# Performance work log

Measured on AMD Instinct MI355X. Metric: run time of the kernel, lower is better.

## Reference

```python
import jax, jax.numpy as jnp
import numpy as np

B, T, E = 4, 2048, 2048
NH, NKV, HD = 16, 4, 128
THETA = 10000.0


def _rope(x, pos_ids, theta):
    # x: [b, h, t, hd]; pos_ids: [b, t]; theta: [hd/2]
    ang = pos_ids[:, None, :, None].astype(jnp.float32) * theta  # [b,1,t,hd/2]
    cos, sin = jnp.cos(ang), jnp.sin(ang)
    x1, x2 = x[..., ::2], x[..., 1::2]
    # interleave rotated pairs back to [..., hd]
    rot = jnp.stack([x1 * cos - x2 * sin, x1 * sin + x2 * cos], axis=-1)
    return rot.reshape(x.shape)


def setup_inputs() -> dict:
    key = jax.random.key(0)
    ks = jax.random.split(key, 10)
    s = 0.02
    x = jax.random.normal(ks[0], (B, T, E), dtype=jnp.float32)
    attention_mask = jax.random.randint(ks[1], (B, T, T), 0, 2, dtype=jnp.int32)
    # torch nn.Linear weights stored here as [in, out] (y = x @ W + b)
    Wq = jax.random.normal(ks[2], (E, E), dtype=jnp.float32) * s
    bq = jnp.zeros((E,), dtype=jnp.float32)
    Wk = jax.random.normal(ks[3], (E, NKV * HD), dtype=jnp.float32) * s
    bk = jnp.zeros((NKV * HD,), dtype=jnp.float32)
    Wv = jax.random.normal(ks[4], (E, NKV * HD), dtype=jnp.float32) * s
    bv = jnp.zeros((NKV * HD,), dtype=jnp.float32)
    Wo = jax.random.normal(ks[5], (E, E), dtype=jnp.float32) * s
    bo = jnp.zeros((E,), dtype=jnp.float32)
    return {"x": x, "attention_mask": attention_mask, "Wq": Wq, "bq": bq,
            "Wk": Wk, "bk": bk, "Wv": Wv, "bv": bv, "Wo": Wo, "bo": bo}


def reference(x, attention_mask, Wq, bq, Wk, bk, Wv, bv, Wo, bo):
    b, t = x.shape[0], x.shape[1]
    # faithful to original: plain reshape (view), NOT transpose-based head split
    q = (x @ Wq + bq).reshape(b, NH, t, HD)
    k = (x @ Wk + bk).reshape(b, NKV, t, HD)
    v = (x @ Wv + bv).reshape(b, NKV, t, HD)
    theta = THETA ** (-jnp.arange(0, HD, 2, dtype=jnp.float32) / HD)
    pos = jnp.broadcast_to(jnp.arange(t), (b, t))
    # original RoPE.forward is wrapped in @torch.no_grad() -> stop_gradient
    k = jax.lax.stop_gradient(_rope(k, pos, theta))
    v = jax.lax.stop_gradient(_rope(v, pos, theta))  # note: RoPE applied to V too
    g = NH // NKV
    k = jnp.tile(k, (1, g, 1, 1))  # torch .repeat tiles kv heads
    v = jnp.tile(v, (1, g, 1, 1))
    # original divides by head_dim ** (-0.5) == multiply by sqrt(head_dim)
    scores = jnp.einsum('bhqd,bhkd->bhqk', q, k) * (HD ** 0.5)
    scores = jnp.where(attention_mask[:, None, :, :] == 0, jnp.float32(1e-9), scores)
    attn = jax.nn.softmax(scores, axis=-1)  # dropout inactive (eval mode)
    out = jnp.einsum('bhqk,bhkd->bhqd', attn, v)
    out = out.transpose(0, 2, 1, 3).reshape(b, t, NH * HD)
    return out @ Wo + bo
```

## Files before the change

kernel.cpp:

```cpp
#include <hip/hip_runtime.h>
#include <math.h>

constexpr int Bc   = 4;
constexpr int Tc   = 2048;
constexpr int Ec   = 2048;
constexpr int NHc  = 16;
constexpr int NKVc = 4;
constexpr int HDc  = 128;
constexpr int KVEc = NKVc * HDc;

typedef __attribute__((ext_vector_type(8))) short bf16x8;
typedef __attribute__((ext_vector_type(4))) short short4v;
typedef __attribute__((ext_vector_type(4))) float f32x4;

__device__ __forceinline__ short f2bf(float f) {
    union { float f; unsigned u; } v; v.f = f;
    unsigned r = v.u + 0x7FFF + ((v.u >> 16) & 1);
    return (short)(r >> 16);
}
__device__ __forceinline__ float bf2f(short s) {
    union { unsigned u; float f; } v; v.u = ((unsigned)(unsigned short)s) << 16;
    return v.f;
}
__device__ __forceinline__ void gload16(const void* g, void* l) {
    __builtin_amdgcn_global_load_lds(
        (const __attribute__((address_space(1))) unsigned*)g,
        (__attribute__((address_space(3))) unsigned*)l, 16, 0, 0);
}

__global__ __launch_bounds__(256)
void convert_split(const float* __restrict__ X, short* __restrict__ Xhi,
                   short* __restrict__ Xlo)
{
    int i = blockIdx.x * 256 + threadIdx.x;
    float4 v = ((const float4*)X)[i];
    float fv[4] = {v.x, v.y, v.z, v.w};
    short4v hi, lo;
    #pragma unroll
    for (int j = 0; j < 4; ++j) {
        hi[j] = f2bf(fv[j]);
        lo[j] = f2bf(fv[j] - bf2f(hi[j]));
    }
    ((short4v*)Xhi)[i] = hi;
    ((short4v*)Xlo)[i] = lo;
}

__global__ __launch_bounds__(256)
void transpose_split(const float* __restrict__ W, short* __restrict__ WThi,
                     short* __restrict__ WTlo, int K, int N)
{
    __shared__ float Ls[32][33];
    const int k0 = blockIdx.x * 32, n0 = blockIdx.y * 32;
    const int t = threadIdx.x;
    const int r = t >> 3, c4 = (t & 7) << 2;
    float4 v = *(const float4*)(W + (size_t)(k0 + r) * N + n0 + c4);
    Ls[r][c4 + 0] = v.x; Ls[r][c4 + 1] = v.y;
    Ls[r][c4 + 2] = v.z; Ls[r][c4 + 3] = v.w;
    __syncthreads();
    short4v hi, lo;
    #pragma unroll
    for (int i = 0; i < 4; ++i) {
        float f = Ls[c4 + i][r];
        hi[i] = f2bf(f);
        lo[i] = f2bf(f - bf2f(hi[i]));
    }
    *(short4v*)(WThi + (size_t)(n0 + r) * K + k0 + c4) = hi;
    if (WTlo) *(short4v*)(WTlo + (size_t)(n0 + r) * K + k0 + c4) = lo;
}

__global__ __launch_bounds__(256)
void mask_bits(const int* __restrict__ mask, unsigned long long* __restrict__ Mb)
{
    const int widx = blockIdx.x * 4 + (threadIdx.x >> 6);
    const int L = threadIdx.x & 63;
    const int m = mask[(size_t)widx * 64 + L];
    unsigned long long bits = __ballot(m != 0);
    if (L == 0) Mb[widx] = bits;
}

template <bool SPLIT>
__global__ __launch_bounds__(256, 2)
void gemm_mfma(const short* __restrict__ Ahi, const short* __restrict__ Alo,
               const short* __restrict__ Bhi, const short* __restrict__ Blo,
               const float* __restrict__ bias, float* __restrict__ C,
               int M, int N, int K)
{
    __shared__ short AsH[128 * 32];
    __shared__ short BsH[128 * 32];
    __shared__ short AsL[SPLIT ? 128 * 32 : 8];
    __shared__ short BsL[SPLIT ? 128 * 32 : 8];

    const int t = threadIdx.x;
    const int w = t >> 6, L = t & 63;
    const int l16 = L & 15, quad = L >> 4;
    const int wr = w >> 1, wc = w & 1;
    const int bm = blockIdx.x * 128, bn = blockIdx.y * 128;

    const int sm = L >> 2;
    const int sq = ((L & 3) - (sm >> 2)) & 3;
    const int scol = sq * 8;

    f32x4 acc[4][4];
    #pragma unroll
    for (int mi = 0; mi < 4; ++mi)
        #pragma unroll
        for (int ni = 0; ni < 4; ++ni) acc[mi][ni] = (f32x4){0, 0, 0, 0};

    const int fxor = (quad + (l16 >> 2)) & 3;

    for (int k0 = 0; k0 < K; k0 += 32) {
        __syncthreads();
        #pragma unroll
        for (int i = 0; i < 2; ++i) {
            const int wl = w * 2 + i;
            const size_t ra = (size_t)(bm + wl * 16 + sm) * K + k0 + scol;
            const size_t rb = (size_t)(bn + wl * 16 + sm) * K + k0 + scol;
            gload16(Ahi + ra, &AsH[wl * 512]);
            gload16(Bhi + rb, &BsH[wl * 512]);
            if (SPLIT) {
                gload16(Alo + ra, &AsL[wl * 512]);
                gload16(Blo + rb, &BsL[wl * 512]);
            }
        }
        __syncthreads();

        bf16x8 ah[4], bh[4], al[4], bl[4];
        #pragma unroll
        for (int mi = 0; mi < 4; ++mi) {
            const int ch = ((wr * 4 + mi) * 64 + l16 * 4 + fxor) * 8;
            ah[mi] = *(const bf16x8*)&AsH[ch];
            if (SPLIT) al[mi] = *(const bf16x8*)&AsL[ch];
        }
        #pragma unroll
        for (int ni = 0; ni < 4; ++ni) {
            const int ch = ((wc * 4 + ni) * 64 + l16 * 4 + fxor) * 8;
            bh[ni] = *(const bf16x8*)&BsH[ch];
            if (SPLIT) bl[ni] = *(const bf16x8*)&BsL[ch];
        }
        #pragma unroll
        for (int mi = 0; mi < 4; ++mi)
            #pragma unroll
            for (int ni = 0; ni < 4; ++ni) {
                acc[mi][ni] = __builtin_amdgcn_mfma_f32_16x16x32_bf16(
                    ah[mi], bh[ni], acc[mi][ni], 0, 0, 0);
                if (SPLIT) {
                    acc[mi][ni] = __builtin_amdgcn_mfma_f32_16x16x32_bf16(
                        al[mi], bh[ni], acc[mi][ni], 0, 0, 0);
                    acc[mi][ni] = __builtin_amdgcn_mfma_f32_16x16x32_bf16(
                        ah[mi], bl[ni], acc[mi][ni], 0, 0, 0);
                }
            }
    }

    #pragma unroll
    for (int ni = 0; ni < 4; ++ni) {
        const int col = bn + wc * 64 + ni * 16 + l16;
        const float bv = bias[col];
        #pragma unroll
        for (int mi = 0; mi < 4; ++mi) {
            #pragma unroll
            for (int r = 0; r < 4; ++r) {
                const int row = bm + wr * 64 + mi * 16 + quad * 4 + r;
                C[(size_t)row * N + col] = acc[mi][ni][r] + bv;
            }
        }
    }
}

__global__ __launch_bounds__(256)
void rope_k(const float* __restrict__ X2d, short* __restrict__ Khi,
            short* __restrict__ Klo)
{
    const int idx = blockIdx.x * 256 + threadIdx.x;
    const int j  = idx & 63;
    const int tk = (idx >> 6) & (Tc - 1);
    const int kh = (idx >> 17) & (NKVc - 1);
    const int bb = idx >> 19;
    const int row = (kh << 9) + (tk >> 2);
    const int col = ((tk & 3) << 7) + (j << 1);
    const float* src = X2d + ((size_t)bb * Tc + row) * KVEc + col;
    const float a = src[0];
    const float b = src[1];
    const float theta = powf(10000.0f, -(float)j * (1.0f / 64.0f));
    const float ang = (float)tk * theta;
    float s, c;
    sincosf(ang, &s, &c);
    const float r0 = a * c - b * s;
    const float r1 = a * s + b * c;
    const size_t off = (((size_t)bb * NKVc + kh) * Tc + tk) * HDc + (j << 1);
    short h0 = f2bf(r0), h1 = f2bf(r1);
    Khi[off]     = h0;  Klo[off]     = f2bf(r0 - bf2f(h0));
    Khi[off + 1] = h1;  Klo[off + 1] = f2bf(r1 - bf2f(h1));
}

__global__ __launch_bounds__(256)
void rope_v_t(const float* __restrict__ V2d, short* __restrict__ Vt)
{
    __shared__ short Ls[128][40];
    const int g  = blockIdx.x;
    const int kh = blockIdx.y;
    const int bb = blockIdx.z;
    const int t  = threadIdx.x;

    const float* src = V2d + ((size_t)bb * Tc + (kh << 9) + (g << 3)) * KVEc;
    #pragma unroll
    for (int i = 0; i < 4; ++i) {
        int e = i * 256 + t;
        float4 v = ((const float4*)src)[e];
        int row = e >> 7;
        int col = (e & 127) << 2;
        int tkl = (row << 2) + (col >> 7);
        int d0  = col & 127;
        int tk  = (g << 5) + tkl;
        float fv[4] = {v.x, v.y, v.z, v.w};
        #pragma unroll
        for (int p = 0; p < 2; ++p) {
            int j = (d0 >> 1) + p;
            float theta = powf(10000.0f, -(float)j * (1.0f / 64.0f));
            float ang = (float)tk * theta;
            float s, c;
            sincosf(ang, &s, &c);
            float a = fv[2 * p], b = fv[2 * p + 1];
            Ls[d0 + 2 * p    ][tkl] = f2bf(a * c - b * s);
            Ls[d0 + 2 * p + 1][tkl] = f2bf(a * s + b * c);
        }
    }
    __syncthreads();
    const int d = t >> 1;
    const int h16 = (t & 1) << 4;
    short* dst = Vt + (((size_t)bb * NKVc + kh) * HDc + d) * Tc + (g << 5) + h16;
    bf16x8 o0 = *(const bf16x8*)&Ls[d][h16];
    bf16x8 o1 = *(const bf16x8*)&Ls[d][h16 + 8];
    *(bf16x8*)dst = o0;
    *(bf16x8*)(dst + 8) = o1;
}

__global__ __launch_bounds__(256, 2)
void attn_mfma(const float* __restrict__ Q2d, const short* __restrict__ Khi_g,
               const short* __restrict__ Klo_g, const short* __restrict__ Vt_g,
               const unsigned long long* __restrict__ Mb, short* __restrict__ AObf)
{
    constexpr int SP = 72;
    __shared__ short KhiS[64 * 128];
    __shared__ short KloS[64 * 128];
    __shared__ short VtS [128 * 64];
    __shared__ short Ps  [64 * SP];

    const int qb = blockIdx.x;
    const int h  = blockIdx.y;
    const int bb = blockIdx.z;
    const int t  = threadIdx.x;
    const int w    = t >> 6;
    const int L    = t & 63;
    const int l16  = L & 15;
    const int quad = L >> 4;
    const int kh   = h & (NKVc - 1);
    const int tq0  = qb * 64 + w * 16;

    bf16x8 qhi[4], qlo[4];
    {
        const float* qrow = Q2d +
            ((size_t)(bb * Tc + h * HDc + qb * 4 + w)) * Ec + 128 * l16;
        #pragma unroll
        for (int kc = 0; kc < 4; ++kc) {
            const float* p = qrow + kc * 32 + quad * 8;
            #pragma unroll
            for (int j = 0; j < 8; ++j) {
                float f = p[j];
                short hi = f2bf(f);
                qhi[kc][j] = hi;
                qlo[kc][j] = f2bf(f - bf2f(hi));
            }
        }
    }

    float m_r[4], lp[4];
    #pragma unroll
    for (int r = 0; r < 4; ++r) { m_r[r] = -INFINITY; lp[r] = 0.0f; }
    f32x4 o[8];
    #pragma unroll
    for (int nc = 0; nc < 8; ++nc) o[nc] = (f32x4){0, 0, 0, 0};

    const short* kbh = Khi_g + ((size_t)(bb * NKVc + kh)) * Tc * HDc;
    const short* kbl = Klo_g + ((size_t)(bb * NKVc + kh)) * Tc * HDc;
    const short* vb  = Vt_g  + ((size_t)(bb * NKVc + kh)) * HDc * Tc;
    const unsigned long long* mrow0 =
        Mb + ((size_t)(bb * Tc + tq0 + quad * 4)) * (Tc / 64);
    const float scale = 11.313708498984761f;

    const int km   = L >> 4;
    const int kpos = L & 15;
    const int vm   = L >> 3;
    const int vc   = ((L & 7) - vm) & 7;

    for (int kt = 0; kt < Tc / 64; ++kt) {
        unsigned long long mw[4];
        #pragma unroll
        for (int r = 0; r < 4; ++r)
            mw[r] = mrow0[(size_t)r * (Tc / 64) + kt];

        __syncthreads();

        #pragma unroll
        for (int i = 0; i < 4; ++i) {
            const int wl = w * 4 + i;
            const int krow = wl * 4 + km;
            const int kc_ = (kpos - (krow & 15)) & 15;
            const size_t go = (size_t)(kt * 64 + krow) * HDc + kc_ * 8;
            gload16(kbh + go, &KhiS[wl * 512]);
            gload16(kbl + go, &KloS[wl * 512]);
            const int vrow = wl * 8 + vm;
            gload16(vb + (size_t)vrow * Tc + kt * 64 + vc * 8, &VtS[wl * 512]);
        }
        __syncthreads();

        f32x4 s[4];
        #pragma unroll
        for (int nt = 0; nt < 4; ++nt) {
            f32x4 acc = (f32x4){0, 0, 0, 0};
            #pragma unroll
            for (int kc = 0; kc < 4; ++kc) {
                const int ch = (((nt * 4 + (l16 >> 2)) << 6) + ((l16 & 3) << 4)
                                + ((kc * 4 + quad + l16) & 15)) << 3;
                bf16x8 khiF = *(const bf16x8*)&KhiS[ch];
                bf16x8 kloF = *(const bf16x8*)&KloS[ch];
                acc = __builtin_amdgcn_mfma_f32_16x16x32_bf16(qhi[kc], khiF, acc, 0, 0, 0);
                acc = __builtin_amdgcn_mfma_f32_16x16x32_bf16(qlo[kc], khiF, acc, 0, 0, 0);
                acc = __builtin_amdgcn_mfma_f32_16x16x32_bf16(qhi[kc], kloF, acc, 0, 0, 0);
            }
            s[nt] = acc;
        }

        #pragma unroll
        for (int r = 0; r < 4; ++r) {
            const unsigned t0 = (unsigned)(mw[r] >> l16);
            const unsigned t1 = (unsigned)(mw[r] >> (l16 + 32));
            s[0][r] = (t0 & 1u)       ? s[0][r] * scale : 1e-9f;
            s[1][r] = (t0 & 0x10000u) ? s[1][r] * scale : 1e-9f;
            s[2][r] = (t1 & 1u)       ? s[2][r] * scale : 1e-9f;
            s[3][r] = (t1 & 0x10000u) ? s[3][r] * scale : 1e-9f;
        }

        float mt[4];
        #pragma unroll
        for (int r = 0; r < 4; ++r)
            mt[r] = fmaxf(fmaxf(s[0][r], s[1][r]), fmaxf(s[2][r], s[3][r]));
        #pragma unroll
        for (int off = 1; off < 16; off <<= 1)
            #pragma unroll
            for (int r = 0; r < 4; ++r)
                mt[r] = fmaxf(mt[r], __shfl_xor(mt[r], off));

        float al[4];
        bool need = false;
        #pragma unroll
        for (int r = 0; r < 4; ++r) {
            const float mn = fmaxf(m_r[r], mt[r]);
            al[r] = __expf(m_r[r] - mn);
            need |= (al[r] < 1.0f);
            m_r[r] = mn;
        }

        float rsum[4];
        #pragma unroll
        for (int r = 0; r < 4; ++r) {
            float p0 = __expf(s[0][r] - m_r[r]);
            float p1 = __expf(s[1][r] - m_r[r]);
            float p2 = __expf(s[2][r] - m_r[r]);
            float p3 = __expf(s[3][r] - m_r[r]);
            s[0][r] = p0; s[1][r] = p1; s[2][r] = p2; s[3][r] = p3;
            rsum[r] = (p0 + p1) + (p2 + p3);
        }

        if (__any(need)) {
            #pragma unroll
            for (int r = 0; r < 4; ++r) lp[r] *= al[r];
            #pragma unroll
            for (int nc = 0; nc < 8; ++nc)
                #pragma unroll
                for (int r = 0; r < 4; ++r)
                    o[nc][r] *= al[r];
        }
        #pragma unroll
        for (int r = 0; r < 4; ++r) lp[r] += rsum[r];

        #pragma unroll
        for (int nt = 0; nt < 4; ++nt)
            #pragma unroll
            for (int r = 0; r < 4; ++r)
                Ps[(w * 16 + quad * 4 + r) * SP + nt * 16 + l16] = f2bf(s[nt][r]);

        bf16x8 a0 = *(const bf16x8*)&Ps[(w * 16 + l16) * SP + quad * 8];
        bf16x8 a1 = *(const bf16x8*)&Ps[(w * 16 + l16) * SP + 32 + quad * 8];

        #pragma unroll
        for (int nc = 0; nc < 8; ++nc) {
            const int rg = (nc * 2 + (l16 >> 3)) << 6;
            const int rm = l16 & 7;
            const int ch0 = (rg + (rm << 3) + ((quad + rm) & 7)) << 3;
            const int ch1 = (rg + (rm << 3) + ((quad + 4 + rm) & 7)) << 3;
            bf16x8 b0 = *(const bf16x8*)&VtS[ch0];
            bf16x8 b1 = *(const bf16x8*)&VtS[ch1];
            o[nc] = __builtin_amdgcn_mfma_f32_16x16x32_bf16(a0, b0, o[nc], 0, 0, 0);
            o[nc] = __builtin_amdgcn_mfma_f32_16x16x32_bf16(a1, b1, o[nc], 0, 0, 0);
        }
    }

    #pragma unroll
    for (int off = 1; off < 16; off <<= 1)
        #pragma unroll
        for (int r = 0; r < 4; ++r)
            lp[r] += __shfl_xor(lp[r], off);

    float inv[4];
    #pragma unroll
    for (int r = 0; r < 4; ++r) inv[r] = 1.0f / lp[r];
    #pragma unroll
    for (int r = 0; r < 4; ++r) {
        short* orow = AObf + ((size_t)(bb * Tc + tq0 + quad * 4 + r)) * Ec
                           + h * HDc + l16;
        #pragma unroll
        for (int nc = 0; nc < 8; ++nc)
            orow[nc * 16] = f2bf(o[nc][r] * inv[r]);
    }
}

extern "C" void kernel_launch(void* const* d_in, const int* in_sizes, int n_in,
                              void* d_out, int out_size, void* d_ws, size_t ws_size,
                              hipStream_t stream)
{
    const float* x    = (const float*)d_in[0];
    const int*  amask = (const int*)  d_in[1];
    const float* Wq   = (const float*)d_in[2];
    const float* bq   = (const float*)d_in[3];
    const float* Wk   = (const float*)d_in[4];
    const float* bk   = (const float*)d_in[5];
    const float* Wv   = (const float*)d_in[6];
    const float* bv   = (const float*)d_in[7];
    const float* Wo   = (const float*)d_in[8];
    const float* bo   = (const float*)d_in[9];
    float* out = (float*)d_out;

    char* ws = (char*)d_ws;
    float* Q2d   = (float*)(ws);
    short* Xhi   = (short*)(ws + 67108864);
    short* Xlo   = (short*)(ws + 100663296);
    short* WqThi = (short*)(ws + 134217728);
    short* WqTlo = (short*)(ws + 134217728 + 8388608);
    float* K2d   = (float*)(ws + 150994944);
    float* V2d   = (float*)(ws + 100663296);
    short* Khi   = (short*)(ws + 100663296 + 16777216);
    short* Klo   = (short*)(ws + 100663296 + 25165824);
    short* WkThi = (short*)(ws + 134217728);
    short* WkTlo = (short*)(ws + 134217728 + 2097152);
    short* WvThi = (short*)(ws + 134217728 + 4194304);
    short* WoThi = (short*)(ws + 134217728 + 8388608);
    short* Vt    = (short*)(ws + 150994944);
    short* AObf  = (short*)(ws + 67108864);
    unsigned long long* Mb = (unsigned long long*)(ws + 167772160);

    const int M = Bc * Tc;
    dim3 blk(256);

    mask_bits<<<(Bc * Tc * (Tc / 64)) / 4, blk, 0, stream>>>(amask, Mb);
    transpose_split<<<dim3(Ec / 32, Ec / 32), blk, 0, stream>>>(Wq, WqThi, WqTlo, Ec, Ec);
    convert_split<<<(M * Ec / 4) / 256, blk, 0, stream>>>(x, Xhi, Xlo);
    gemm_mfma<true><<<dim3(M / 128, Ec / 128), blk, 0, stream>>>(
        Xhi, Xlo, WqThi, WqTlo, bq, Q2d, M, Ec, Ec);
    transpose_split<<<dim3(Ec / 32, KVEc / 32), blk, 0, stream>>>(Wk, WkThi, WkTlo, Ec, KVEc);
    transpose_split<<<dim3(Ec / 32, KVEc / 32), blk, 0, stream>>>(Wv, WvThi, nullptr, Ec, KVEc);
    transpose_split<<<dim3(Ec / 32, Ec / 32), blk, 0, stream>>>(Wo, WoThi, nullptr, Ec, Ec);
    gemm_mfma<true><<<dim3(M / 128, KVEc / 128), blk, 0, stream>>>(
        Xhi, Xlo, WkThi, WkTlo, bk, K2d, M, KVEc, Ec);
    gemm_mfma<false><<<dim3(M / 128, KVEc / 128), blk, 0, stream>>>(
        Xhi, nullptr, WvThi, nullptr, bv, V2d, M, KVEc, Ec);
    rope_k<<<(Bc * NKVc * Tc * 64) / 256, blk, 0, stream>>>(K2d, Khi, Klo);
    rope_v_t<<<dim3(Tc / 32, NKVc, Bc), blk, 0, stream>>>(V2d, Vt);
    attn_mfma<<<dim3(Tc / 64, NHc, Bc), blk, 0, stream>>>(
        Q2d, Khi, Klo, Vt, Mb, AObf);
    gemm_mfma<false><<<dim3(M / 128, Ec / 128), blk, 0, stream>>>(
        AObf, nullptr, WoThi, nullptr, bo, out, M, Ec, Ec);
}
```

Baseline: 1.030 ms.

## Transpose QK MFMA, keep P in registers via shuffles, use exp2 and setprio

Swaps the MFMA operands so each lane holds one query column's scores. That lets the softmax row max and sum use two cross-quad shuffles instead of four-step reductions, with one scalar max and sum per lane. The P tile is packed to bf16 with v_cvt_pk_bf16_f32 and redistributed through lane shuffles instead of a round trip through LDS, so the Ps shared buffer goes away. Exponentials use raw v_exp_f32 with the log2(e) factor folded into the scale. The change also adds s_setprio around the MFMA phases, remaps block ids so blocks sharing a KV head run together, and raises launch bounds to 3 blocks per CU, at the cost of more shuffle traffic and register pressure.

```diff
diff --git a/kernel.cpp b/kernel.cpp
--- a/kernel.cpp
+++ b/kernel.cpp
@@ -21,6 +21,9 @@
 __device__ __forceinline__ float bf2f(short s) {
     union { unsigned u; float f; } v; v.u = ((unsigned)(unsigned short)s) << 16;
     return v.f;
+}
+__device__ __forceinline__ float ex2(float x) {
+    float r; asm("v_exp_f32 %0, %1" : "=v"(r) : "v"(x)); return r;
 }
 __device__ __forceinline__ void gload16(const void* g, void* l) {
     __builtin_amdgcn_global_load_lds(
@@ -235,25 +238,28 @@
     *(bf16x8*)(dst + 8) = o1;
 }
 
-__global__ __launch_bounds__(256, 2)
+__global__ __launch_bounds__(256, 3)
 void attn_mfma(const float* __restrict__ Q2d, const short* __restrict__ Khi_g,
                const short* __restrict__ Klo_g, const short* __restrict__ Vt_g,
                const unsigned long long* __restrict__ Mb, short* __restrict__ AObf)
 {
-    constexpr int SP = 72;
     __shared__ short KhiS[64 * 128];
     __shared__ short KloS[64 * 128];
     __shared__ short VtS [128 * 64];
-    __shared__ short Ps  [64 * SP];
-
-    const int qb = blockIdx.x;
-    const int h  = blockIdx.y;
-    const int bb = blockIdx.z;
-    const int t  = threadIdx.x;
+
+    const int fid  = blockIdx.x + 32 * (blockIdx.y + 16 * blockIdx.z);
+    const int slot = fid >> 3;
+    const int grp  = (fid & 7) + 8 * (slot >> 5);
+    const int qb   = slot & 31;
+    const int h    = grp & 15;
+    const int bb   = grp >> 4;
+
+    const int t    = threadIdx.x;
     const int w    = t >> 6;
     const int L    = t & 63;
     const int l16  = L & 15;
     const int quad = L >> 4;
+    const int q1v  = quad >> 1;
     const int kh   = h & (NKVc - 1);
     const int tq0  = qb * 64 + w * 16;
 
@@ -274,9 +280,7 @@
         }
     }
 
-    float m_r[4], lp[4];
-    #pragma unroll
-    for (int r = 0; r < 4; ++r) { m_r[r] = -INFINITY; lp[r] = 0.0f; }
+    float m_r = -INFINITY, lp = 0.0f;
     f32x4 o[8];
     #pragma unroll
     for (int nc = 0; nc < 8; ++nc) o[nc] = (f32x4){0, 0, 0, 0};
@@ -284,20 +288,22 @@
     const short* kbh = Khi_g + ((size_t)(bb * NKVc + kh)) * Tc * HDc;
     const short* kbl = Klo_g + ((size_t)(bb * NKVc + kh)) * Tc * HDc;
     const short* vb  = Vt_g  + ((size_t)(bb * NKVc + kh)) * HDc * Tc;
-    const unsigned long long* mrow0 =
-        Mb + ((size_t)(bb * Tc + tq0 + quad * 4)) * (Tc / 64);
-    const float scale = 11.313708498984761f;
+    const unsigned long long* mrow =
+        Mb + ((size_t)(bb * Tc + tq0 + l16)) * (Tc / 64);
+
+    constexpr float SCALE2  = 11.313708498984761f * 1.4426950408889634f;
+    constexpr float MASKED2 = 1e-9f * 1.4426950408889634f;
 
     const int km   = L >> 4;
     const int kpos = L & 15;
     const int vm   = L >> 3;
     const int vc   = ((L & 7) - vm) & 7;
 
+    const int srcA = l16 + 16 * ((2 * quad)     & 3);
+    const int srcB = l16 + 16 * ((2 * quad + 1) & 3);
+
     for (int kt = 0; kt < Tc / 64; ++kt) {
-        unsigned long long mw[4];
-        #pragma unroll
-        for (int r = 0; r < 4; ++r)
-            mw[r] = mrow0[(size_t)r * (Tc / 64) + kt];
+        const unsigned long long mw = mrow[kt];
 
         __syncthreads();
 
@@ -315,6 +321,7 @@
         __syncthreads();
 
         f32x4 s[4];
+        __builtin_amdgcn_s_setprio(1);
         #pragma unroll
         for (int nt = 0; nt < 4; ++nt) {
             f32x4 acc = (f32x4){0, 0, 0, 0};
@@ -324,75 +331,92 @@
                                 + ((kc * 4 + quad + l16) & 15)) << 3;
                 bf16x8 khiF = *(const bf16x8*)&KhiS[ch];
                 bf16x8 kloF = *(const bf16x8*)&KloS[ch];
-                acc = __builtin_amdgcn_mfma_f32_16x16x32_bf16(qhi[kc], khiF, acc, 0, 0, 0);
-                acc = __builtin_amdgcn_mfma_f32_16x16x32_bf16(qlo[kc], khiF, acc, 0, 0, 0);
-                acc = __builtin_amdgcn_mfma_f32_16x16x32_bf16(qhi[kc], kloF, acc, 0, 0, 0);
+                acc = __builtin_amdgcn_mfma_f32_16x16x32_bf16(khiF, qhi[kc], acc, 0, 0, 0);
+                acc = __builtin_amdgcn_mfma_f32_16x16x32_bf16(khiF, qlo[kc], acc, 0, 0, 0);
+                acc = __builtin_amdgcn_mfma_f32_16x16x32_bf16(kloF, qhi[kc], acc, 0, 0, 0);
             }
             s[nt] = acc;
         }
-
-        #pragma unroll
-        for (int r = 0; r < 4; ++r) {
-            const unsigned t0 = (unsigned)(mw[r] >> l16);
-            const unsigned t1 = (unsigned)(mw[r] >> (l16 + 32));
-            s[0][r] = (t0 & 1u)       ? s[0][r] * scale : 1e-9f;
-            s[1][r] = (t0 & 0x10000u) ? s[1][r] * scale : 1e-9f;
-            s[2][r] = (t1 & 1u)       ? s[2][r] * scale : 1e-9f;
-            s[3][r] = (t1 & 0x10000u) ? s[3][r] * scale : 1e-9f;
-        }
-
-        float mt[4];
-        #pragma unroll
-        for (int r = 0; r < 4; ++r)
-            mt[r] = fmaxf(fmaxf(s[0][r], s[1][r]), fmaxf(s[2][r], s[3][r]));
-        #pragma unroll
-        for (int off = 1; off < 16; off <<= 1)
+        __builtin_amdgcn_s_setprio(0);
+
+        const unsigned mlo = (unsigned)mw;
+        const unsigned mhi = (unsigned)(mw >> 32);
+        const int gq = quad << 2;
+        const unsigned fm[4] = { mlo >> gq, (mlo >> 16) >> gq,
+                                 mhi >> gq, (mhi >> 16) >> gq };
+        #pragma unroll
+        for (int nt = 0; nt < 4; ++nt)
             #pragma unroll
             for (int r = 0; r < 4; ++r)
-                mt[r] = fmaxf(mt[r], __shfl_xor(mt[r], off));
-
-        float al[4];
-        bool need = false;
-        #pragma unroll
-        for (int r = 0; r < 4; ++r) {
-            const float mn = fmaxf(m_r[r], mt[r]);
-            al[r] = __expf(m_r[r] - mn);
-            need |= (al[r] < 1.0f);
-            m_r[r] = mn;
-        }
-
-        float rsum[4];
-        #pragma unroll
-        for (int r = 0; r < 4; ++r) {
-            float p0 = __expf(s[0][r] - m_r[r]);
-            float p1 = __expf(s[1][r] - m_r[r]);
-            float p2 = __expf(s[2][r] - m_r[r]);
-            float p3 = __expf(s[3][r] - m_r[r]);
-            s[0][r] = p0; s[1][r] = p1; s[2][r] = p2; s[3][r] = p3;
-            rsum[r] = (p0 + p1) + (p2 + p3);
-        }
-
-        if (__any(need)) {
-            #pragma unroll
-            for (int r = 0; r < 4; ++r) lp[r] *= al[r];
+                s[nt][r] = (fm[nt] & (1u << r)) ? s[nt][r] * SCALE2 : MASKED2;
+
+        float mt;
+        {
+            float a0 = fmaxf(fmaxf(s[0][0], s[0][1]), fmaxf(s[0][2], s[0][3]));
+            float a1 = fmaxf(fmaxf(s[1][0], s[1][1]), fmaxf(s[1][2], s[1][3]));
+            float a2 = fmaxf(fmaxf(s[2][0], s[2][1]), fmaxf(s[2][2], s[2][3]));
+            float a3 = fmaxf(fmaxf(s[3][0], s[3][1]), fmaxf(s[3][2], s[3][3]));
+            mt = fmaxf(fmaxf(a0, a1), fmaxf(a2, a3));
+        }
+        mt = fmaxf(mt, __shfl_xor(mt, 16));
+        mt = fmaxf(mt, __shfl_xor(mt, 32));
+        const float mn  = fmaxf(m_r, mt);
+        const float alq = ex2(m_r - mn);
+        m_r = mn;
+
+        float rs;
+        {
+            float t0 = 0.f, t1 = 0.f;
+            #pragma unroll
+            for (int nt = 0; nt < 4; ++nt) {
+                float p0 = ex2(s[nt][0] - mn);
+                float p1 = ex2(s[nt][1] - mn);
+                float p2 = ex2(s[nt][2] - mn);
+                float p3 = ex2(s[nt][3] - mn);
+                s[nt][0] = p0; s[nt][1] = p1; s[nt][2] = p2; s[nt][3] = p3;
+                t0 += p0 + p1; t1 += p2 + p3;
+            }
+            rs = t0 + t1;
+        }
+
+        if (__any(alq < 1.0f)) {
+            lp *= alq;
+            float alo[4];
+            #pragma unroll
+            for (int r = 0; r < 4; ++r)
+                alo[r] = __shfl(alq, quad * 16 + quad * 4 + r);
             #pragma unroll
             for (int nc = 0; nc < 8; ++nc)
                 #pragma unroll
                 for (int r = 0; r < 4; ++r)
-                    o[nc][r] *= al[r];
-        }
-        #pragma unroll
-        for (int r = 0; r < 4; ++r) lp[r] += rsum[r];
-
-        #pragma unroll
-        for (int nt = 0; nt < 4; ++nt)
-            #pragma unroll
-            for (int r = 0; r < 4; ++r)
-                Ps[(w * 16 + quad * 4 + r) * SP + nt * 16 + l16] = f2bf(s[nt][r]);
-
-        bf16x8 a0 = *(const bf16x8*)&Ps[(w * 16 + l16) * SP + quad * 8];
-        bf16x8 a1 = *(const bf16x8*)&Ps[(w * 16 + l16) * SP + 32 + quad * 8];
-
+                    o[nc][r] *= alo[r];
+        }
+        lp += rs;
+
+        int pk00, pk01, pk10, pk11, pk20, pk21, pk30, pk31;
+        asm("v_cvt_pk_bf16_f32 %0, %1, %2" : "=v"(pk00) : "v"(s[0][0]), "v"(s[0][1]));
+        asm("v_cvt_pk_bf16_f32 %0, %1, %2" : "=v"(pk01) : "v"(s[0][2]), "v"(s[0][3]));
+        asm("v_cvt_pk_bf16_f32 %0, %1, %2" : "=v"(pk10) : "v"(s[1][0]), "v"(s[1][1]));
+        asm("v_cvt_pk_bf16_f32 %0, %1, %2" : "=v"(pk11) : "v"(s[1][2]), "v"(s[1][3]));
+        asm("v_cvt_pk_bf16_f32 %0, %1, %2" : "=v"(pk20) : "v"(s[2][0]), "v"(s[2][1]));
+        asm("v_cvt_pk_bf16_f32 %0, %1, %2" : "=v"(pk21) : "v"(s[2][2]), "v"(s[2][3]));
+        asm("v_cvt_pk_bf16_f32 %0, %1, %2" : "=v"(pk30) : "v"(s[3][0]), "v"(s[3][1]));
+        asm("v_cvt_pk_bf16_f32 %0, %1, %2" : "=v"(pk31) : "v"(s[3][2]), "v"(s[3][3]));
+
+        union U { int d[4]; bf16x8 v; } A0, A1;
+        {
+            int u0, u1;
+            u0 = __shfl(pk00, srcA); u1 = __shfl(pk10, srcA); A0.d[0] = q1v ? u1 : u0;
+            u0 = __shfl(pk01, srcA); u1 = __shfl(pk11, srcA); A0.d[1] = q1v ? u1 : u0;
+            u0 = __shfl(pk00, srcB); u1 = __shfl(pk10, srcB); A0.d[2] = q1v ? u1 : u0;
+            u0 = __shfl(pk01, srcB); u1 = __shfl(pk11, srcB); A0.d[3] = q1v ? u1 : u0;
+            u0 = __shfl(pk20, srcA); u1 = __shfl(pk30, srcA); A1.d[0] = q1v ? u1 : u0;
+            u0 = __shfl(pk21, srcA); u1 = __shfl(pk31, srcA); A1.d[1] = q1v ? u1 : u0;
+            u0 = __shfl(pk20, srcB); u1 = __shfl(pk30, srcB); A1.d[2] = q1v ? u1 : u0;
+            u0 = __shfl(pk21, srcB); u1 = __shfl(pk31, srcB); A1.d[3] = q1v ? u1 : u0;
+        }
+
+        __builtin_amdgcn_s_setprio(1);
         #pragma unroll
         for (int nc = 0; nc < 8; ++nc) {
             const int rg = (nc * 2 + (l16 >> 3)) << 6;
@@ -401,27 +425,27 @@
             const int ch1 = (rg + (rm << 3) + ((quad + 4 + rm) & 7)) << 3;
             bf16x8 b0 = *(const bf16x8*)&VtS[ch0];
             bf16x8 b1 = *(const bf16x8*)&VtS[ch1];
-            o[nc] = __builtin_amdgcn_mfma_f32_16x16x32_bf16(a0, b0, o[nc], 0, 0, 0);
-            o[nc] = __builtin_amdgcn_mfma_f32_16x16x32_bf16(a1, b1, o[nc], 0, 0, 0);
-        }
-    }
-
-    #pragma unroll
-    for (int off = 1; off < 16; off <<= 1)
-        #pragma unroll
-        for (int r = 0; r < 4; ++r)
-            lp[r] += __shfl_xor(lp[r], off);
-
-    float inv[4];
-    #pragma unroll
-    for (int r = 0; r < 4; ++r) inv[r] = 1.0f / lp[r];
+            o[nc] = __builtin_amdgcn_mfma_f32_16x16x32_bf16(A0.v, b0, o[nc], 0, 0, 0);
+            o[nc] = __builtin_amdgcn_mfma_f32_16x16x32_bf16(A1.v, b1, o[nc], 0, 0, 0);
+        }
+        __builtin_amdgcn_s_setprio(0);
+    }
+
+    lp += __shfl_xor(lp, 16);
+    lp += __shfl_xor(lp, 32);
+    const float invl = 1.0f / lp;
+    float invo[4];
+    #pragma unroll
+    for (int r = 0; r < 4; ++r)
+        invo[r] = __shfl(invl, quad * 16 + quad * 4 + r);
+
     #pragma unroll
     for (int r = 0; r < 4; ++r) {
         short* orow = AObf + ((size_t)(bb * Tc + tq0 + quad * 4 + r)) * Ec
                            + h * HDc + l16;
         #pragma unroll
         for (int nc = 0; nc < 8; ++nc)
-            orow[nc * 16] = f2bf(o[nc][r] * inv[r]);
+            orow[nc * 16] = f2bf(o[nc][r] * invo[r]);
     }
 }
 
```

After: 1.127 ms. 1.09x slower.
